# Optimization experiments

Measured on AMD Instinct MI355X. Metric: run time of the kernel, lower is better.

Reference implementation:

```python
import jax, jax.numpy as jnp
import numpy as np

EPS = 1e-8  # torch F.cosine_similarity default eps


def setup_inputs() -> dict:
    key0 = jax.random.key(0)
    k1, k2, k3, k4 = jax.random.split(key0, 4)
    B, H, K, D = 8, 16, 2048, 128
    query = jax.random.normal(k1, (B, H, 1, D), dtype=jnp.float32)
    key = jax.random.normal(k2, (B, H, K, D), dtype=jnp.float32)
    value = jax.random.normal(k3, (B, H, K, D), dtype=jnp.float32)
    mask = jax.random.randint(k4, (B, K), 0, 2, dtype=jnp.int32)
    return {"query": query, "key": key, "value": value, "mask": mask}


def reference(query, key, value, mask):
    # Cosine similarity along the feature dim without materializing the
    # repeated query tensor: broadcast the single query vector per (b, h).
    q_norm = jnp.maximum(jnp.linalg.norm(query, axis=-1), EPS)  # [B, H, 1]
    k_norm = jnp.maximum(jnp.linalg.norm(key, axis=-1), EPS)    # [B, H, K]
    dot = jnp.einsum('bhod,bhkd->bhk', query, key)              # o == 1
    scores = jnp.abs(dot / (q_norm * k_norm))                   # [B, H, K]
    # mask [B, K] -> broadcast over heads; masked positions -> -1e9
    scores = jnp.where(mask[:, None, :] == 0, jnp.float32(-1e9), scores)
    p_attn = jnp.exp(scores)                                    # [B, H, K]
    out = p_attn[:, :, :, None] * value                         # [B, H, K, D]
    return (out, p_attn)
```

## Files before the change

kernel.cpp:

```cpp
#include <hip/hip_runtime.h>
#include <math.h>

#define EPS 1e-8f

constexpr int B = 8, H = 16, K = 2048, D = 128;
constexpr int BH = B * H;
constexpr int SPLIT = 16;
constexpr int ROWS_PER_CHUNK = K / SPLIT;
constexpr int WAVES = 4;
constexpr int SLOTS = WAVES * 2;
constexpr int ROWS_PER_SLOT = ROWS_PER_CHUNK / SLOTS;
constexpr int GROUP = 4;
constexpr int NGROUPS = ROWS_PER_SLOT / GROUP;
constexpr size_t P_OFF = (size_t)BH * K * D;

typedef float f32x4 __attribute__((ext_vector_type(4)));

__global__ __launch_bounds__(256) void cosattn_kernel(
    const float* __restrict__ q,
    const float* __restrict__ key,
    const float* __restrict__ value,
    const int*   __restrict__ mask,
    float* __restrict__ out)
{
    const int tid  = threadIdx.x;
    const int lane = tid & 63;
    const int half = lane >> 5;
    const int l32  = lane & 31;
    const int wave = tid >> 6;
    const int slot = wave * 2 + half;

    const int bh    = blockIdx.x / SPLIT;
    const int chunk = blockIdx.x % SPLIT;
    const int b     = bh / H;

    const f32x4 qv = *reinterpret_cast<const f32x4*>(q + (size_t)bh * D + l32 * 4);
    float qsq = qv[0]*qv[0] + qv[1]*qv[1] + qv[2]*qv[2] + qv[3]*qv[3];
    #pragma unroll
    for (int s = 16; s >= 1; s >>= 1)
        qsq += __shfl_xor(qsq, s, 64);
    const float inv_qn = 1.0f / fmaxf(sqrtf(qsq), EPS);

    const int row0 = chunk * ROWS_PER_CHUNK;

    int mk = 0;
    if (l32 < ROWS_PER_SLOT)
        mk = mask[b * K + row0 + l32 * SLOTS + slot];
    const unsigned long long bal = __ballot(mk != 0);
    const unsigned bits = (unsigned)(bal >> (half * 32)) & 0xFFFFu;

    const size_t baseRow = (size_t)bh * K;

    #pragma unroll 1
    for (int g = 0; g < NGROUPS; ++g) {
        int   r[GROUP];
        bool  act[GROUP];
        f32x4 kv[GROUP], vv[GROUP];

        #pragma unroll
        for (int j = 0; j < GROUP; ++j) {
            const int i = g * GROUP + j;
            r[j]   = row0 + i * SLOTS + slot;
            act[j] = (bits >> i) & 1u;
            const size_t off = (baseRow + r[j]) * D + l32 * 4;
            kv[j] = act[j] ? *reinterpret_cast<const f32x4*>(key + off)
                           : (f32x4)(0.0f);
            vv[j] = act[j] ? *reinterpret_cast<const f32x4*>(value + off)
                           : (f32x4)(0.0f);
        }

        float dot[GROUP], ksq[GROUP];
        #pragma unroll
        for (int j = 0; j < GROUP; ++j) {
            dot[j] = qv[0]*kv[j][0] + qv[1]*kv[j][1] + qv[2]*kv[j][2] + qv[3]*kv[j][3];
            ksq[j] = kv[j][0]*kv[j][0] + kv[j][1]*kv[j][1] + kv[j][2]*kv[j][2] + kv[j][3]*kv[j][3];
        }
        #pragma unroll
        for (int s = 16; s >= 1; s >>= 1) {
            #pragma unroll
            for (int j = 0; j < GROUP; ++j) {
                dot[j] += __shfl_xor(dot[j], s, 64);
                ksq[j] += __shfl_xor(ksq[j], s, 64);
            }
        }

        #pragma unroll
        for (int j = 0; j < GROUP; ++j) {
            const float kn_inv = 1.0f / fmaxf(sqrtf(ksq[j]), EPS);
            const float p = act[j] ? expf(fabsf(dot[j]) * inv_qn * kn_inv) : 0.0f;
            f32x4 ov;
            ov[0] = p * vv[j][0];
            ov[1] = p * vv[j][1];
            ov[2] = p * vv[j][2];
            ov[3] = p * vv[j][3];
            const size_t off = (baseRow + r[j]) * D + l32 * 4;
            __builtin_nontemporal_store(ov, reinterpret_cast<f32x4*>(out + off));
            if (l32 == 0)
                __builtin_nontemporal_store(p, out + P_OFF + baseRow + r[j]);
        }
    }
}

extern "C" void kernel_launch(void* const* d_in, const int* in_sizes, int n_in,
                              void* d_out, int out_size, void* d_ws, size_t ws_size,
                              hipStream_t stream) {
    const float* q   = (const float*)d_in[0];
    const float* key = (const float*)d_in[1];
    const float* val = (const float*)d_in[2];
    const int*   msk = (const int*)d_in[3];
    float* out = (float*)d_out;

    dim3 grid(BH * SPLIT);
    dim3 block(WAVES * 64);
    cosattn_kernel<<<grid, block, 0, stream>>>(q, key, val, msk, out);
}
```

Before: 45.44 us.

## Double-buffer key/value loads, contiguous slot rows, coalesced p_attn store

Each half-wave slot now owns a contiguous run of rows instead of rows strided by SLOTS, and the next group's key/value loads are issued before the current group is computed, with the loop fully unrolled. The per-row scalar p_attn stores are replaced by one coalesced store per slot at the end, and expf becomes __expf. The aim is to hide memory latency and reduce scattered small stores, at the cost of more registers from the double buffer and a slightly less accurate exp.

```diff
diff --git a/kernel.cpp b/kernel.cpp
--- a/kernel.cpp
+++ b/kernel.cpp
@@ -41,39 +41,47 @@
         qsq += __shfl_xor(qsq, s, 64);
     const float inv_qn = 1.0f / fmaxf(sqrtf(qsq), EPS);
 
-    const int row0 = chunk * ROWS_PER_CHUNK;
+    const int slotBase = chunk * ROWS_PER_CHUNK + slot * ROWS_PER_SLOT;
+    const size_t baseRow = (size_t)bh * K;
 
     int mk = 0;
     if (l32 < ROWS_PER_SLOT)
-        mk = mask[b * K + row0 + l32 * SLOTS + slot];
+        mk = mask[b * K + slotBase + l32];
     const unsigned long long bal = __ballot(mk != 0);
     const unsigned bits = (unsigned)(bal >> (half * 32)) & 0xFFFFu;
 
-    const size_t baseRow = (size_t)bh * K;
+    const float* kbase = key   + (baseRow + slotBase) * D + l32 * 4;
+    const float* vbase = value + (baseRow + slotBase) * D + l32 * 4;
+    float*       obase = out   + (baseRow + slotBase) * D + l32 * 4;
 
-    #pragma unroll 1
+    f32x4 kvb[2][GROUP], vvb[2][GROUP];
+
+    #define LOADG(g, buf)                                                     \
+        _Pragma("unroll")                                                     \
+        for (int j = 0; j < GROUP; ++j) {                                     \
+            const int i = (g) * GROUP + j;                                    \
+            const bool a = (bits >> i) & 1u;                                  \
+            kvb[buf][j] = a ? *reinterpret_cast<const f32x4*>(kbase + i * D)  \
+                            : (f32x4)(0.0f);                                  \
+            vvb[buf][j] = a ? *reinterpret_cast<const f32x4*>(vbase + i * D)  \
+                            : (f32x4)(0.0f);                                  \
+        }
+
+    float myp = 0.0f;
+
+    LOADG(0, 0);
+
+    #pragma unroll
     for (int g = 0; g < NGROUPS; ++g) {
-        int   r[GROUP];
-        bool  act[GROUP];
-        f32x4 kv[GROUP], vv[GROUP];
-
-        #pragma unroll
-        for (int j = 0; j < GROUP; ++j) {
-            const int i = g * GROUP + j;
-            r[j]   = row0 + i * SLOTS + slot;
-            act[j] = (bits >> i) & 1u;
-            const size_t off = (baseRow + r[j]) * D + l32 * 4;
-            kv[j] = act[j] ? *reinterpret_cast<const f32x4*>(key + off)
-                           : (f32x4)(0.0f);
-            vv[j] = act[j] ? *reinterpret_cast<const f32x4*>(value + off)
-                           : (f32x4)(0.0f);
-        }
+        const int buf = g & 1;
+        if (g + 1 < NGROUPS) { LOADG(g + 1, buf ^ 1); }
 
         float dot[GROUP], ksq[GROUP];
         #pragma unroll
         for (int j = 0; j < GROUP; ++j) {
-            dot[j] = qv[0]*kv[j][0] + qv[1]*kv[j][1] + qv[2]*kv[j][2] + qv[3]*kv[j][3];
-            ksq[j] = kv[j][0]*kv[j][0] + kv[j][1]*kv[j][1] + kv[j][2]*kv[j][2] + kv[j][3]*kv[j][3];
+            const f32x4 kv = kvb[buf][j];
+            dot[j] = qv[0]*kv[0] + qv[1]*kv[1] + qv[2]*kv[2] + qv[3]*kv[3];
+            ksq[j] = kv[0]*kv[0] + kv[1]*kv[1] + kv[2]*kv[2] + kv[3]*kv[3];
         }
         #pragma unroll
         for (int s = 16; s >= 1; s >>= 1) {
@@ -83,22 +91,24 @@
                 ksq[j] += __shfl_xor(ksq[j], s, 64);
             }
         }
-
         #pragma unroll
         for (int j = 0; j < GROUP; ++j) {
+            const int i = g * GROUP + j;
+            const bool a = (bits >> i) & 1u;
             const float kn_inv = 1.0f / fmaxf(sqrtf(ksq[j]), EPS);
-            const float p = act[j] ? expf(fabsf(dot[j]) * inv_qn * kn_inv) : 0.0f;
+            const float p = a ? __expf(fabsf(dot[j]) * inv_qn * kn_inv) : 0.0f;
+            if (l32 == i) myp = p;
+            const f32x4 vv = vvb[buf][j];
             f32x4 ov;
-            ov[0] = p * vv[j][0];
-            ov[1] = p * vv[j][1];
-            ov[2] = p * vv[j][2];
-            ov[3] = p * vv[j][3];
-            const size_t off = (baseRow + r[j]) * D + l32 * 4;
-            __builtin_nontemporal_store(ov, reinterpret_cast<f32x4*>(out + off));
-            if (l32 == 0)
-                __builtin_nontemporal_store(p, out + P_OFF + baseRow + r[j]);
+            ov[0] = p * vv[0]; ov[1] = p * vv[1];
+            ov[2] = p * vv[2]; ov[3] = p * vv[3];
+            __builtin_nontemporal_store(ov, reinterpret_cast<f32x4*>(obase + i * D));
         }
     }
+    #undef LOADG
+
+    if (l32 < ROWS_PER_SLOT)
+        __builtin_nontemporal_store(myp, out + P_OFF + baseRow + slotBase + l32);
 }
 
 extern "C" void kernel_launch(void* const* d_in, const int* in_sizes, int n_in,
```

After: 46.49 us. 2.3% more time.

## Use many small blocks with contiguous rows and hoisted loads

Applied to the files above, without the earlier changes.

Each block now covers 32 contiguous rows instead of 128 strided ones, so the grid grows fourfold and the group loop goes away. Each half-wave owns 4 consecutive rows, and all of its key and value loads are issued before any compute. The p values are coalesced into one store per lane instead of one scalar store per row, and expf is replaced by the faster __expf. The aim is more memory-level parallelism and contiguous access for this bandwidth-bound kernel, at the cost of more block launches and some extra per-block setup (q norm and mask load repeated per block).

```diff
diff --git a/kernel.cpp b/kernel.cpp
--- a/kernel.cpp
+++ b/kernel.cpp
@@ -5,13 +5,11 @@
 
 constexpr int B = 8, H = 16, K = 2048, D = 128;
 constexpr int BH = B * H;
-constexpr int SPLIT = 16;
-constexpr int ROWS_PER_CHUNK = K / SPLIT;
+constexpr int ROWS_PER_BLOCK = 32;
+constexpr int CHUNKS = K / ROWS_PER_BLOCK;
 constexpr int WAVES = 4;
 constexpr int SLOTS = WAVES * 2;
-constexpr int ROWS_PER_SLOT = ROWS_PER_CHUNK / SLOTS;
-constexpr int GROUP = 4;
-constexpr int NGROUPS = ROWS_PER_SLOT / GROUP;
+constexpr int RPS = ROWS_PER_BLOCK / SLOTS;
 constexpr size_t P_OFF = (size_t)BH * K * D;
 
 typedef float f32x4 __attribute__((ext_vector_type(4)));
@@ -30,75 +28,71 @@
     const int wave = tid >> 6;
     const int slot = wave * 2 + half;
 
-    const int bh    = blockIdx.x / SPLIT;
-    const int chunk = blockIdx.x % SPLIT;
+    const int bh    = blockIdx.x >> 6;
+    const int chunk = blockIdx.x & (CHUNKS - 1);
     const int b     = bh / H;
 
+    const int slotBase = chunk * ROWS_PER_BLOCK + slot * RPS;
+    const size_t baseRow = (size_t)bh * K;
+
+    int mk = 0;
+    if (l32 < RPS)
+        mk = mask[b * K + slotBase + l32];
+    const unsigned long long bal = __ballot(mk != 0);
+    const unsigned bits = (unsigned)(bal >> (half * 32)) & 0xFu;
+
     const f32x4 qv = *reinterpret_cast<const f32x4*>(q + (size_t)bh * D + l32 * 4);
+
+    const float* kbase = key   + (baseRow + slotBase) * D + l32 * 4;
+    const float* vbase = value + (baseRow + slotBase) * D + l32 * 4;
+    float*       obase = out   + (baseRow + slotBase) * D + l32 * 4;
+
+    f32x4 kv[RPS], vv[RPS];
+    #pragma unroll
+    for (int j = 0; j < RPS; ++j)
+        kv[j] = ((bits >> j) & 1u) ? *reinterpret_cast<const f32x4*>(kbase + j * D)
+                                   : (f32x4)(0.0f);
+    #pragma unroll
+    for (int j = 0; j < RPS; ++j)
+        vv[j] = ((bits >> j) & 1u) ? *reinterpret_cast<const f32x4*>(vbase + j * D)
+                                   : (f32x4)(0.0f);
+
     float qsq = qv[0]*qv[0] + qv[1]*qv[1] + qv[2]*qv[2] + qv[3]*qv[3];
     #pragma unroll
     for (int s = 16; s >= 1; s >>= 1)
         qsq += __shfl_xor(qsq, s, 64);
     const float inv_qn = 1.0f / fmaxf(sqrtf(qsq), EPS);
 
-    const int row0 = chunk * ROWS_PER_CHUNK;
-
-    int mk = 0;
-    if (l32 < ROWS_PER_SLOT)
-        mk = mask[b * K + row0 + l32 * SLOTS + slot];
-    const unsigned long long bal = __ballot(mk != 0);
-    const unsigned bits = (unsigned)(bal >> (half * 32)) & 0xFFFFu;
-
-    const size_t baseRow = (size_t)bh * K;
-
-    #pragma unroll 1
-    for (int g = 0; g < NGROUPS; ++g) {
-        int   r[GROUP];
-        bool  act[GROUP];
-        f32x4 kv[GROUP], vv[GROUP];
-
+    float dot[RPS], ksq[RPS];
+    #pragma unroll
+    for (int j = 0; j < RPS; ++j) {
+        dot[j] = qv[0]*kv[j][0] + qv[1]*kv[j][1] + qv[2]*kv[j][2] + qv[3]*kv[j][3];
+        ksq[j] = kv[j][0]*kv[j][0] + kv[j][1]*kv[j][1] + kv[j][2]*kv[j][2] + kv[j][3]*kv[j][3];
+    }
+    #pragma unroll
+    for (int s = 16; s >= 1; s >>= 1) {
         #pragma unroll
-        for (int j = 0; j < GROUP; ++j) {
-            const int i = g * GROUP + j;
-            r[j]   = row0 + i * SLOTS + slot;
-            act[j] = (bits >> i) & 1u;
-            const size_t off = (baseRow + r[j]) * D + l32 * 4;
-            kv[j] = act[j] ? *reinterpret_cast<const f32x4*>(key + off)
-                           : (f32x4)(0.0f);
-            vv[j] = act[j] ? *reinterpret_cast<const f32x4*>(value + off)
-                           : (f32x4)(0.0f);
-        }
-
-        float dot[GROUP], ksq[GROUP];
-        #pragma unroll
-        for (int j = 0; j < GROUP; ++j) {
-            dot[j] = qv[0]*kv[j][0] + qv[1]*kv[j][1] + qv[2]*kv[j][2] + qv[3]*kv[j][3];
-            ksq[j] = kv[j][0]*kv[j][0] + kv[j][1]*kv[j][1] + kv[j][2]*kv[j][2] + kv[j][3]*kv[j][3];
-        }
-        #pragma unroll
-        for (int s = 16; s >= 1; s >>= 1) {
-            #pragma unroll
-            for (int j = 0; j < GROUP; ++j) {
-                dot[j] += __shfl_xor(dot[j], s, 64);
-                ksq[j] += __shfl_xor(ksq[j], s, 64);
-            }
-        }
-
-        #pragma unroll
-        for (int j = 0; j < GROUP; ++j) {
-            const float kn_inv = 1.0f / fmaxf(sqrtf(ksq[j]), EPS);
-            const float p = act[j] ? expf(fabsf(dot[j]) * inv_qn * kn_inv) : 0.0f;
-            f32x4 ov;
-            ov[0] = p * vv[j][0];
-            ov[1] = p * vv[j][1];
-            ov[2] = p * vv[j][2];
-            ov[3] = p * vv[j][3];
-            const size_t off = (baseRow + r[j]) * D + l32 * 4;
-            __builtin_nontemporal_store(ov, reinterpret_cast<f32x4*>(out + off));
-            if (l32 == 0)
-                __builtin_nontemporal_store(p, out + P_OFF + baseRow + r[j]);
+        for (int j = 0; j < RPS; ++j) {
+            dot[j] += __shfl_xor(dot[j], s, 64);
+            ksq[j] += __shfl_xor(ksq[j], s, 64);
         }
     }
+
+    float myp = 0.0f;
+    #pragma unroll
+    for (int j = 0; j < RPS; ++j) {
+        const bool a = (bits >> j) & 1u;
+        const float kn_inv = 1.0f / fmaxf(sqrtf(ksq[j]), EPS);
+        const float p = a ? __expf(fabsf(dot[j]) * inv_qn * kn_inv) : 0.0f;
+        if (l32 == j) myp = p;
+        f32x4 ov;
+        ov[0] = p * vv[j][0]; ov[1] = p * vv[j][1];
+        ov[2] = p * vv[j][2]; ov[3] = p * vv[j][3];
+        __builtin_nontemporal_store(ov, reinterpret_cast<f32x4*>(obase + j * D));
+    }
+
+    if (l32 < RPS)
+        __builtin_nontemporal_store(myp, out + P_OFF + baseRow + slotBase + l32);
 }
 
 extern "C" void kernel_launch(void* const* d_in, const int* in_sizes, int n_in,
@@ -110,7 +104,7 @@
     const int*   msk = (const int*)d_in[3];
     float* out = (float*)d_out;
 
-    dim3 grid(BH * SPLIT);
+    dim3 grid(BH * CHUNKS);
     dim3 block(WAVES * 64);
     cosattn_kernel<<<grid, block, 0, stream>>>(q, key, val, msk, out);
 }
```

Result: faster. 43.03 us (median of 2 runs) (-5.3%).
